# Optimization experiments

Hardware: AMD Instinct MI355X
Metric: run time of the kernel (lower is better)

The kernel has to match this reference:

```python
import jax, jax.numpy as jnp
import numpy as np

B, IN_F, OUT_F = 4096, 4096, 11008  # tokens, in_features, out_features


def setup_inputs() -> dict:
    key = jax.random.key(0)
    k1, k2, k3, k4 = jax.random.split(key, 4)
    x = jax.random.normal(k1, (B, IN_F), dtype=jnp.float32)
    # Each int holds two packed 4-bit codes (low nibble = even col, high nibble = odd col).
    packed_weights = jax.random.randint(k2, (OUT_F, IN_F // 2), 0, 256, dtype=jnp.int32)
    scales = jax.random.uniform(k3, (OUT_F,), dtype=jnp.float32) * 0.02 + 1e-4
    zero_points = jax.random.uniform(k4, (OUT_F,), dtype=jnp.float32) * 15.0
    return {"x": x, "packed_weights": packed_weights, "scales": scales,
            "zero_points": zero_points}


def _dequantize(packed_weights, scales, zero_points):
    # Unpack two 4-bit codes per byte -> q: [OUT_F, IN_F]
    low = (packed_weights & 15).astype(jnp.float32)
    high = ((packed_weights >> 4) & 15).astype(jnp.float32)
    q = jnp.stack([low, high], axis=-1).reshape(packed_weights.shape[0], -1)
    # Per-row affine dequant: w = (q - zero_point) * scale
    return (q - zero_points[:, None]) * scales[:, None]


def reference(x, packed_weights, scales, zero_points):
    W = _dequantize(packed_weights, scales, zero_points)  # [OUT_F, IN_F]
    return x @ W.T  # [B, OUT_F]
```

## Files before the change

kernel.cpp:

```cpp
#include <hip/hip_runtime.h>
#include <hip/hip_bf16.h>
#include <stdint.h>

#define M_DIM 4096
#define N_DIM 11008
#define K_DIM 4096
#define KP    (K_DIM / 2)

typedef __attribute__((ext_vector_type(4))) int i32x4;

#define AS1 __attribute__((address_space(1)))
#define AS3 __attribute__((address_space(3)))

__global__ __launch_bounds__(256) void pack_q(const int* __restrict__ pw,
                                              signed char* __restrict__ wq) {
  const int total = (N_DIM * KP) / 4;
  for (int i = blockIdx.x * 256 + threadIdx.x; i < total; i += gridDim.x * 256) {
    int4 p = ((const int4*)pw)[i];
    int v[4] = {p.x, p.y, p.z, p.w};
    unsigned int u0 = 0, u1 = 0;
#pragma unroll
    for (int j = 0; j < 2; ++j) {
      unsigned int b0 = (unsigned int)(2 * (v[j] & 15) - 15) & 0xFF;
      unsigned int b1 = (unsigned int)(2 * ((v[j] >> 4) & 15) - 15) & 0xFF;
      u0 |= (b0 | (b1 << 8)) << (16 * j);
    }
#pragma unroll
    for (int j = 0; j < 2; ++j) {
      unsigned int b0 = (unsigned int)(2 * (v[2 + j] & 15) - 15) & 0xFF;
      unsigned int b1 = (unsigned int)(2 * ((v[2 + j] >> 4) & 15) - 15) & 0xFF;
      u1 |= (b0 | (b1 << 8)) << (16 * j);
    }
    uint2 st; st.x = u0; st.y = u1;
    ((uint2*)wq)[i] = st;
  }
}

__global__ __launch_bounds__(256) void quant_x(const float* __restrict__ x,
                                               signed char* __restrict__ xq,
                                               float* __restrict__ r,
                                               float* __restrict__ sx) {
  const int row = blockIdx.x;
  const int t = threadIdx.x;
  const int lane = t & 63, wid = t >> 6;
  const float4* x4 = (const float4*)(x + (size_t)row * K_DIM);
  float4 v[4];
  float am = 0.0f, sm = 0.0f;
#pragma unroll
  for (int i = 0; i < 4; ++i) {
    v[i] = x4[i * 256 + t];
    sm += v[i].x + v[i].y + v[i].z + v[i].w;
    am = fmaxf(am, fmaxf(fmaxf(fabsf(v[i].x), fabsf(v[i].y)),
                         fmaxf(fabsf(v[i].z), fabsf(v[i].w))));
  }
#pragma unroll
  for (int off = 32; off >= 1; off >>= 1) {
    am = fmaxf(am, __shfl_xor(am, off));
    sm += __shfl_xor(sm, off);
  }
  __shared__ float smax[4], ssum[4];
  if (lane == 0) { smax[wid] = am; ssum[wid] = sm; }
  __syncthreads();
  am = fmaxf(fmaxf(smax[0], smax[1]), fmaxf(smax[2], smax[3]));
  sm = ssum[0] + ssum[1] + ssum[2] + ssum[3];
  const float inv = am > 0.0f ? 127.0f / am : 0.0f;
  unsigned int* xo = (unsigned int*)(xq + (size_t)row * K_DIM);
#pragma unroll
  for (int i = 0; i < 4; ++i) {
    int q0 = min(127, max(-127, __float2int_rn(v[i].x * inv)));
    int q1 = min(127, max(-127, __float2int_rn(v[i].y * inv)));
    int q2 = min(127, max(-127, __float2int_rn(v[i].z * inv)));
    int q3 = min(127, max(-127, __float2int_rn(v[i].w * inv)));
    xo[i * 256 + t] = ((unsigned int)q0 & 0xFF) | (((unsigned int)q1 & 0xFF) << 8) |
                      (((unsigned int)q2 & 0xFF) << 16) | (((unsigned int)q3 & 0xFF) << 24);
  }
  if (t == 0) { r[row] = sm; sx[row] = am > 0.0f ? am / 127.0f : 0.0f; }
}

#define BM 256
#define BN 256
#define BK 128
#define NTILE (K_DIM / BK)
#define NT_M (M_DIM / BM)
#define NT_N (N_DIM / BN)
#define NWG  (NT_M * NT_N)
#define HS 16384
#define PS 65536

#define WAITV(n) asm volatile("s_waitcnt vmcnt(" #n ")" ::: "memory")
#define WAITL0   asm volatile("s_waitcnt lgkmcnt(0)" ::: "memory")
#define BARR     do { asm volatile("" ::: "memory"); __builtin_amdgcn_s_barrier(); asm volatile("" ::: "memory"); } while (0)

__global__ __launch_bounds__(512, 2) void gemm_i8(const signed char* __restrict__ Xq,
                                                  const signed char* __restrict__ Wq,
                                                  const float* __restrict__ sc,
                                                  const float* __restrict__ zp,
                                                  const float* __restrict__ rbuf,
                                                  const float* __restrict__ sxbuf,
                                                  float* __restrict__ C) {
  __shared__ __align__(16) unsigned char lds8[131072];

  const int t = threadIdx.x;
  const int bid = blockIdx.x;
  const int swz = (bid & 7) * (NWG / 8) + (bid >> 3);
  const int tm = swz & 15;
  const int tn = swz >> 4;

  const int srow = t >> 3;
  const int g0 = (t & 7) ^ (srow & 7);
  const int koff = g0 * 16;
  const signed char* pB0c0 = Wq + (size_t)(tn * BN + srow) * K_DIM + koff;
  const signed char* pB0c1 = Wq + (size_t)(tn * BN + 64 + srow) * K_DIM + koff;
  const signed char* pB1c0 = Wq + (size_t)(tn * BN + 128 + srow) * K_DIM + koff;
  const signed char* pB1c1 = Wq + (size_t)(tn * BN + 192 + srow) * K_DIM + koff;
  const signed char* pA0c0 = Xq + (size_t)(tm * BM + srow) * K_DIM + koff;
  const signed char* pA0c1 = Xq + (size_t)(tm * BM + 64 + srow) * K_DIM + koff;
  const signed char* pA1c0 = Xq + (size_t)(tm * BM + 128 + srow) * K_DIM + koff;
  const signed char* pA1c1 = Xq + (size_t)(tm * BM + 192 + srow) * K_DIM + koff;
  const int d0 = t * 16;
  const int d1 = d0 + 8192;

  const int lane = t & 63;
  const int w = t >> 6;
  const int wm = w >> 2;
  const int wn = w & 3;
  const int lr = lane & 15, lk = lane >> 4;

  const int j0 = lk ^ (lr & 7);
  const int aB0 = (2 + wm) * HS + lr * 128 + j0 * 16;
  const int aB1 = aB0 ^ 64;
  const int bB0 = (wn >> 1) * HS + (wn & 1) * 8192 + lr * 128 + j0 * 16;
  const int bB1 = bB0 ^ 64;

  i32x4 acc[8][4] = {};

#define GLL(src, dstoff) \
  __builtin_amdgcn_global_load_lds((const AS1 void*)(src), (AS3 void*)(lds8 + (dstoff)), 16, 0, 0)

  GLL(pB0c0, 0 * HS + d0); GLL(pB0c1, 0 * HS + d1);
  GLL(pB1c0, 1 * HS + d0); GLL(pB1c1, 1 * HS + d1);
  GLL(pA0c0, 2 * HS + d0); GLL(pA0c1, 2 * HS + d1);
  GLL(pA1c0, 3 * HS + d0); GLL(pA1c1, 3 * HS + d1);
  GLL(pB0c0 + BK, 4 * HS + d0); GLL(pB0c1 + BK, 4 * HS + d1);
  GLL(pB1c0 + BK, 5 * HS + d0); GLL(pB1c1 + BK, 5 * HS + d1);
  pB0c0 += 2 * BK; pB0c1 += 2 * BK; pB1c0 += 2 * BK; pB1c1 += 2 * BK;
  pA0c0 += BK;     pA0c1 += BK;     pA1c0 += BK;     pA1c1 += BK;
  WAITV(4);
  BARR;

#define TILE(P, SA, SB, VMODE) do {                                                        \
    i32x4 af[4], bf0[4], bf1[4];                                                           \
                               \
    _Pragma("unroll") for (int i = 0; i < 4; ++i)                                          \
      af[i] = *(const i32x4*)(lds8 + (P) * PS + aB0 + i * 2048);                           \
    _Pragma("unroll") for (int n = 0; n < 4; ++n)                                          \
      bf0[n] = *(const i32x4*)(lds8 + (P) * PS + bB0 + n * 2048);                          \
    if (SA) { GLL(pA0c0, (((P) ^ 1) * 4 + 2) * HS + d0);                                   \
              GLL(pA0c1, (((P) ^ 1) * 4 + 2) * HS + d1);                                   \
              pA0c0 += BK; pA0c1 += BK; }                                                  \
    __builtin_amdgcn_s_setprio(1);                                                         \
    _Pragma("unroll") for (int i = 0; i < 4; ++i)                                          \
      _Pragma("unroll") for (int n = 0; n < 4; ++n)                                        \
        acc[i][n] = __builtin_amdgcn_mfma_i32_16x16x64_i8(af[i], bf0[n], acc[i][n], 0, 0, 0); \
    __builtin_amdgcn_s_setprio(0);                                                         \
      \
    _Pragma("unroll") for (int i = 0; i < 4; ++i)                                          \
      af[i] = *(const i32x4*)(lds8 + (P) * PS + aB0 + (4 + i) * 2048);                     \
    _Pragma("unroll") for (int n = 0; n < 4; ++n)                                          \
      bf1[n] = *(const i32x4*)(lds8 + (P) * PS + bB1 + n * 2048);                          \
    if (SA) { GLL(pA1c0, (((P) ^ 1) * 4 + 3) * HS + d0);                                   \
              GLL(pA1c1, (((P) ^ 1) * 4 + 3) * HS + d1);                                   \
              pA1c0 += BK; pA1c1 += BK; }                                                  \
    __builtin_amdgcn_s_setprio(1);                                                         \
    _Pragma("unroll") for (int i = 0; i < 4; ++i)                                          \
      _Pragma("unroll") for (int n = 0; n < 4; ++n)                                        \
        acc[4 + i][n] = __builtin_amdgcn_mfma_i32_16x16x64_i8(af[i], bf0[n], acc[4 + i][n], 0, 0, 0); \
    __builtin_amdgcn_s_setprio(0);                                                         \
    WAITL0;                                                                                \
    BARR;                                                                                  \
                                  \
    _Pragma("unroll") for (int i = 0; i < 4; ++i)                                          \
      af[i] = *(const i32x4*)(lds8 + (P) * PS + aB1 + i * 2048);                           \
    if (SB) { GLL(pB0c0, ((P) * 4 + 0) * HS + d0);                                         \
              GLL(pB0c1, ((P) * 4 + 0) * HS + d1);                                         \
              pB0c0 += BK; pB0c1 += BK; }                                                  \
    __builtin_amdgcn_s_setprio(1);                                                         \
    _Pragma("unroll") for (int i = 0; i < 4; ++i)                                          \
      _Pragma("unroll") for (int n = 0; n < 4; ++n)                                        \
        acc[i][n] = __builtin_amdgcn_mfma_i32_16x16x64_i8(af[i], bf1[n], acc[i][n], 0, 0, 0); \
    __builtin_amdgcn_s_setprio(0);                                                         \
              \
    _Pragma("unroll") for (int i = 0; i < 4; ++i)                                          \
      af[i] = *(const i32x4*)(lds8 + (P) * PS + aB1 + (4 + i) * 2048);                     \
    if (SB) { GLL(pB1c0, ((P) * 4 + 1) * HS + d0);                                         \
              GLL(pB1c1, ((P) * 4 + 1) * HS + d1);                                         \
              pB1c0 += BK; pB1c1 += BK; }                                                  \
    __builtin_amdgcn_s_setprio(1);                                                         \
    _Pragma("unroll") for (int i = 0; i < 4; ++i)                                          \
      _Pragma("unroll") for (int n = 0; n < 4; ++n)                                        \
        acc[4 + i][n] = __builtin_amdgcn_mfma_i32_16x16x64_i8(af[i], bf1[n], acc[4 + i][n], 0, 0, 0); \
    __builtin_amdgcn_s_setprio(0);                                                         \
    if ((VMODE) == 0) { WAITV(4); } else if ((VMODE) == 1) { WAITV(0); }                   \
    BARR;                                                                                  \
  } while (0)

  for (int it = 0; it < (NTILE - 2) / 2; ++it) {
    TILE(0, 1, 1, 0);
    TILE(1, 1, 1, 0);
  }
  TILE(0, 1, 0, 1);
  TILE(1, 0, 0, 2);

#undef TILE
#undef GLL

  const int row0 = tm * BM + wm * 128 + lk * 4;
  const int col0 = tn * BN + wn * 64 + lr;
  float sv[4], zv[4];
#pragma unroll
  for (int n = 0; n < 4; ++n) {
    sv[n] = sc[col0 + n * 16];
    zv[n] = 7.5f - zp[col0 + n * 16];
  }
#pragma unroll
  for (int m = 0; m < 8; ++m)
#pragma unroll
    for (int rr = 0; rr < 4; ++rr) {
      const int row = row0 + m * 16 + rr;
      const float rv = rbuf[row];
      const float hx = 0.5f * sxbuf[row];
#pragma unroll
      for (int n = 0; n < 4; ++n)
        C[(size_t)row * N_DIM + col0 + n * 16] = sv[n] * (hx * (float)acc[m][n][rr] + zv[n] * rv);
    }
}

__global__ __launch_bounds__(256) void fallback_gemm(const float* __restrict__ x,
                                                     const int* __restrict__ pw,
                                                     const float* __restrict__ sc,
                                                     const float* __restrict__ zp,
                                                     float* __restrict__ out) {
  __shared__ float Xs[64][33];
  __shared__ float Ws[64][33];
  const int bid = blockIdx.x;
  const int bm = bid & 63;
  const int bn = bid >> 6;
  const int t = threadIdx.x;
  const int tx = t & 15, ty = t >> 4;
  float acc[4][4] = {};
  for (int k0 = 0; k0 < K_DIM; k0 += 32) {
    __syncthreads();
#pragma unroll
    for (int i = 0; i < 8; ++i) {
      int e = t + i * 256; int r = e >> 5, c = e & 31;
      Xs[r][c] = x[(size_t)(bm * 64 + r) * K_DIM + k0 + c];
    }
#pragma unroll
    for (int i = 0; i < 4; ++i) {
      int e = t + i * 256; int rr = e >> 4, jj = e & 15;
      int row = bn * 64 + rr;
      int v = pw[(size_t)row * KP + (k0 >> 1) + jj];
      float s = sc[row], z = zp[row];
      Ws[rr][2 * jj]     = ((float)(v & 15) - z) * s;
      Ws[rr][2 * jj + 1] = ((float)((v >> 4) & 15) - z) * s;
    }
    __syncthreads();
#pragma unroll
    for (int kk = 0; kk < 32; ++kk) {
      float a[4], b[4];
#pragma unroll
      for (int i2 = 0; i2 < 4; ++i2) a[i2] = Xs[ty * 4 + i2][kk];
#pragma unroll
      for (int j2 = 0; j2 < 4; ++j2) b[j2] = Ws[tx * 4 + j2][kk];
#pragma unroll
      for (int i2 = 0; i2 < 4; ++i2)
#pragma unroll
        for (int j2 = 0; j2 < 4; ++j2) acc[i2][j2] += a[i2] * b[j2];
    }
  }
#pragma unroll
  for (int i2 = 0; i2 < 4; ++i2)
#pragma unroll
    for (int j2 = 0; j2 < 4; ++j2)
      out[(size_t)(bm * 64 + ty * 4 + i2) * N_DIM + bn * 64 + tx * 4 + j2] = acc[i2][j2];
}

extern "C" void kernel_launch(void* const* d_in, const int* in_sizes, int n_in,
                              void* d_out, int out_size, void* d_ws, size_t ws_size,
                              hipStream_t stream) {
  const float* x  = (const float*)d_in[0];
  const int*   pw = (const int*)d_in[1];
  const float* sc = (const float*)d_in[2];
  const float* zp = (const float*)d_in[3];
  float* out = (float*)d_out;

  const size_t wq_b = (size_t)N_DIM * K_DIM;
  const size_t xq_b = (size_t)M_DIM * K_DIM;
  const size_t need = wq_b + xq_b + 2 * 4096 * sizeof(float);

  if (ws_size >= need) {
    signed char* wq = (signed char*)d_ws;
    signed char* xq = wq + wq_b;
    float* rbuf  = (float*)((char*)d_ws + wq_b + xq_b);
    float* sxbuf = rbuf + 4096;
    hipLaunchKernelGGL(pack_q,  dim3(2048), dim3(256), 0, stream, pw, wq);
    hipLaunchKernelGGL(quant_x, dim3(4096), dim3(256), 0, stream, x, xq, rbuf, sxbuf);
    hipLaunchKernelGGL(gemm_i8, dim3(NWG),  dim3(512), 0, stream, xq, wq, sc, zp, rbuf, sxbuf, out);
  } else {
    hipLaunchKernelGGL(fallback_gemm, dim3(64 * 172), dim3(256), 0, stream, x, pw, sc, zp, out);
  }
}
```

Before: 225.2 us.

## Shrink GEMM tiles to 256x128x64 with triple-buffered LDS and fuse prep kernels

Merges the weight-repack and activation-quantize kernels into one launch, splitting the grid into two block ranges. Restructures the int8 MFMA GEMM from 256x256x128 double-buffered tiles to 256x128x64 tiles with a three-stage LDS ring, a new XOR swizzle and a simpler single-phase tile body. The goal is higher occupancy (launch bounds raised to 4 and a smaller LDS footprint) and deeper load pipelining. The cost is lower arithmetic intensity per tile, more global traffic for A, and twice as many workgroups.

```diff
diff --git a/kernel.cpp b/kernel.cpp
--- a/kernel.cpp
+++ b/kernel.cpp
@@ -12,93 +12,95 @@
 #define AS1 __attribute__((address_space(1)))
 #define AS3 __attribute__((address_space(3)))
 
-__global__ __launch_bounds__(256) void pack_q(const int* __restrict__ pw,
-                                              signed char* __restrict__ wq) {
-  const int total = (N_DIM * KP) / 4;
-  for (int i = blockIdx.x * 256 + threadIdx.x; i < total; i += gridDim.x * 256) {
-    int4 p = ((const int4*)pw)[i];
-    int v[4] = {p.x, p.y, p.z, p.w};
-    unsigned int u0 = 0, u1 = 0;
-#pragma unroll
-    for (int j = 0; j < 2; ++j) {
-      unsigned int b0 = (unsigned int)(2 * (v[j] & 15) - 15) & 0xFF;
-      unsigned int b1 = (unsigned int)(2 * ((v[j] >> 4) & 15) - 15) & 0xFF;
-      u0 |= (b0 | (b1 << 8)) << (16 * j);
-    }
-#pragma unroll
-    for (int j = 0; j < 2; ++j) {
-      unsigned int b0 = (unsigned int)(2 * (v[2 + j] & 15) - 15) & 0xFF;
-      unsigned int b1 = (unsigned int)(2 * ((v[2 + j] >> 4) & 15) - 15) & 0xFF;
-      u1 |= (b0 | (b1 << 8)) << (16 * j);
-    }
-    uint2 st; st.x = u0; st.y = u1;
-    ((uint2*)wq)[i] = st;
-  }
-}
-
-__global__ __launch_bounds__(256) void quant_x(const float* __restrict__ x,
-                                               signed char* __restrict__ xq,
-                                               float* __restrict__ r,
-                                               float* __restrict__ sx) {
-  const int row = blockIdx.x;
+__global__ __launch_bounds__(256) void prep(const float* __restrict__ x,
+                                            const int* __restrict__ pw,
+                                            signed char* __restrict__ xq,
+                                            signed char* __restrict__ wq,
+                                            float* __restrict__ r,
+                                            float* __restrict__ sx) {
+  const int b = blockIdx.x;
   const int t = threadIdx.x;
-  const int lane = t & 63, wid = t >> 6;
-  const float4* x4 = (const float4*)(x + (size_t)row * K_DIM);
-  float4 v[4];
-  float am = 0.0f, sm = 0.0f;
-#pragma unroll
-  for (int i = 0; i < 4; ++i) {
-    v[i] = x4[i * 256 + t];
-    sm += v[i].x + v[i].y + v[i].z + v[i].w;
-    am = fmaxf(am, fmaxf(fmaxf(fabsf(v[i].x), fabsf(v[i].y)),
-                         fmaxf(fabsf(v[i].z), fabsf(v[i].w))));
-  }
-#pragma unroll
-  for (int off = 32; off >= 1; off >>= 1) {
-    am = fmaxf(am, __shfl_xor(am, off));
-    sm += __shfl_xor(sm, off);
-  }
-  __shared__ float smax[4], ssum[4];
-  if (lane == 0) { smax[wid] = am; ssum[wid] = sm; }
-  __syncthreads();
-  am = fmaxf(fmaxf(smax[0], smax[1]), fmaxf(smax[2], smax[3]));
-  sm = ssum[0] + ssum[1] + ssum[2] + ssum[3];
-  const float inv = am > 0.0f ? 127.0f / am : 0.0f;
-  unsigned int* xo = (unsigned int*)(xq + (size_t)row * K_DIM);
-#pragma unroll
-  for (int i = 0; i < 4; ++i) {
-    int q0 = min(127, max(-127, __float2int_rn(v[i].x * inv)));
-    int q1 = min(127, max(-127, __float2int_rn(v[i].y * inv)));
-    int q2 = min(127, max(-127, __float2int_rn(v[i].z * inv)));
-    int q3 = min(127, max(-127, __float2int_rn(v[i].w * inv)));
-    xo[i * 256 + t] = ((unsigned int)q0 & 0xFF) | (((unsigned int)q1 & 0xFF) << 8) |
-                      (((unsigned int)q2 & 0xFF) << 16) | (((unsigned int)q3 & 0xFF) << 24);
-  }
-  if (t == 0) { r[row] = sm; sx[row] = am > 0.0f ? am / 127.0f : 0.0f; }
+  if (b < 4096) {
+    const int row = b;
+    const int lane = t & 63, wid = t >> 6;
+    const float4* x4 = (const float4*)(x + (size_t)row * K_DIM);
+    float4 v[4];
+    float am = 0.0f, sm = 0.0f;
+#pragma unroll
+    for (int i = 0; i < 4; ++i) {
+      v[i] = x4[i * 256 + t];
+      sm += v[i].x + v[i].y + v[i].z + v[i].w;
+      am = fmaxf(am, fmaxf(fmaxf(fabsf(v[i].x), fabsf(v[i].y)),
+                           fmaxf(fabsf(v[i].z), fabsf(v[i].w))));
+    }
+#pragma unroll
+    for (int off = 32; off >= 1; off >>= 1) {
+      am = fmaxf(am, __shfl_xor(am, off));
+      sm += __shfl_xor(sm, off);
+    }
+    __shared__ float smax[4], ssum[4];
+    if (lane == 0) { smax[wid] = am; ssum[wid] = sm; }
+    __syncthreads();
+    am = fmaxf(fmaxf(smax[0], smax[1]), fmaxf(smax[2], smax[3]));
+    sm = ssum[0] + ssum[1] + ssum[2] + ssum[3];
+    const float inv = am > 0.0f ? 127.0f / am : 0.0f;
+    unsigned int* xo = (unsigned int*)(xq + (size_t)row * K_DIM);
+#pragma unroll
+    for (int i = 0; i < 4; ++i) {
+      int q0 = min(127, max(-127, __float2int_rn(v[i].x * inv)));
+      int q1 = min(127, max(-127, __float2int_rn(v[i].y * inv)));
+      int q2 = min(127, max(-127, __float2int_rn(v[i].z * inv)));
+      int q3 = min(127, max(-127, __float2int_rn(v[i].w * inv)));
+      xo[i * 256 + t] = ((unsigned int)q0 & 0xFF) | (((unsigned int)q1 & 0xFF) << 8) |
+                        (((unsigned int)q2 & 0xFF) << 16) | (((unsigned int)q3 & 0xFF) << 24);
+    }
+    if (t == 0) { r[row] = sm; sx[row] = am > 0.0f ? am / 127.0f : 0.0f; }
+  } else {
+    const int total = (N_DIM * KP) / 4;
+    for (int i = (b - 4096) * 256 + t; i < total; i += 2048 * 256) {
+      int4 p = ((const int4*)pw)[i];
+      int v[4] = {p.x, p.y, p.z, p.w};
+      unsigned int u0 = 0, u1 = 0;
+#pragma unroll
+      for (int j = 0; j < 2; ++j) {
+        unsigned int b0 = (unsigned int)(2 * (v[j] & 15) - 15) & 0xFF;
+        unsigned int b1 = (unsigned int)(2 * ((v[j] >> 4) & 15) - 15) & 0xFF;
+        u0 |= (b0 | (b1 << 8)) << (16 * j);
+      }
+#pragma unroll
+      for (int j = 0; j < 2; ++j) {
+        unsigned int b0 = (unsigned int)(2 * (v[2 + j] & 15) - 15) & 0xFF;
+        unsigned int b1 = (unsigned int)(2 * ((v[2 + j] >> 4) & 15) - 15) & 0xFF;
+        u1 |= (b0 | (b1 << 8)) << (16 * j);
+      }
+      uint2 st; st.x = u0; st.y = u1;
+      ((uint2*)wq)[i] = st;
+    }
+  }
 }
 
 #define BM 256
-#define BN 256
-#define BK 128
+#define BN 128
+#define BK 64
 #define NTILE (K_DIM / BK)
 #define NT_M (M_DIM / BM)
 #define NT_N (N_DIM / BN)
 #define NWG  (NT_M * NT_N)
-#define HS 16384
-#define PS 65536
+#define SLOT 8192
+#define PAR  24576
 
 #define WAITV(n) asm volatile("s_waitcnt vmcnt(" #n ")" ::: "memory")
 #define WAITL0   asm volatile("s_waitcnt lgkmcnt(0)" ::: "memory")
 #define BARR     do { asm volatile("" ::: "memory"); __builtin_amdgcn_s_barrier(); asm volatile("" ::: "memory"); } while (0)
 
-__global__ __launch_bounds__(512, 2) void gemm_i8(const signed char* __restrict__ Xq,
+__global__ __launch_bounds__(512, 4) void gemm_i8(const signed char* __restrict__ Xq,
                                                   const signed char* __restrict__ Wq,
                                                   const float* __restrict__ sc,
                                                   const float* __restrict__ zp,
                                                   const float* __restrict__ rbuf,
                                                   const float* __restrict__ sxbuf,
                                                   float* __restrict__ C) {
-  __shared__ __align__(16) unsigned char lds8[131072];
+  __shared__ __align__(16) unsigned char lds8[73728];
 
   const int t = threadIdx.x;
   const int bid = blockIdx.x;
@@ -106,115 +108,76 @@
   const int tm = swz & 15;
   const int tn = swz >> 4;
 
-  const int srow = t >> 3;
-  const int g0 = (t & 7) ^ (srow & 7);
+  const int srow = t >> 2;
+  const int g0 = (t & 3) ^ (srow & 3) ^ ((srow >> 2) & 3);
   const int koff = g0 * 16;
-  const signed char* pB0c0 = Wq + (size_t)(tn * BN + srow) * K_DIM + koff;
-  const signed char* pB0c1 = Wq + (size_t)(tn * BN + 64 + srow) * K_DIM + koff;
-  const signed char* pB1c0 = Wq + (size_t)(tn * BN + 128 + srow) * K_DIM + koff;
-  const signed char* pB1c1 = Wq + (size_t)(tn * BN + 192 + srow) * K_DIM + koff;
-  const signed char* pA0c0 = Xq + (size_t)(tm * BM + srow) * K_DIM + koff;
-  const signed char* pA0c1 = Xq + (size_t)(tm * BM + 64 + srow) * K_DIM + koff;
-  const signed char* pA1c0 = Xq + (size_t)(tm * BM + 128 + srow) * K_DIM + koff;
-  const signed char* pA1c1 = Xq + (size_t)(tm * BM + 192 + srow) * K_DIM + koff;
-  const int d0 = t * 16;
-  const int d1 = d0 + 8192;
+  const signed char* pB  = Wq + (size_t)(tn * BN + srow) * K_DIM + koff;
+  const signed char* pA0 = Xq + (size_t)(tm * BM + srow) * K_DIM + koff;
+  const signed char* pA1 = Xq + (size_t)(tm * BM + 128 + srow) * K_DIM + koff;
+  const int d = t * 16;
 
   const int lane = t & 63;
   const int w = t >> 6;
-  const int wm = w >> 2;
-  const int wn = w & 3;
+  const int wm = w >> 1;
+  const int wn = w & 1;
   const int lr = lane & 15, lk = lane >> 4;
 
-  const int j0 = lk ^ (lr & 7);
-  const int aB0 = (2 + wm) * HS + lr * 128 + j0 * 16;
-  const int aB1 = aB0 ^ 64;
-  const int bB0 = (wn >> 1) * HS + (wn & 1) * 8192 + lr * 128 + j0 * 16;
-  const int bB1 = bB0 ^ 64;
-
-  i32x4 acc[8][4] = {};
+  const int js = lk ^ (lr & 3) ^ ((lr >> 2) & 3);
+  const int aBase = (1 + (wm >> 1)) * SLOT + ((wm & 1) * 64 + lr) * 64 + js * 16;
+  const int bBase = (wn * 64 + lr) * 64 + js * 16;
+
+  i32x4 acc[4][4] = {};
 
 #define GLL(src, dstoff) \
   __builtin_amdgcn_global_load_lds((const AS1 void*)(src), (AS3 void*)(lds8 + (dstoff)), 16, 0, 0)
 
-  GLL(pB0c0, 0 * HS + d0); GLL(pB0c1, 0 * HS + d1);
-  GLL(pB1c0, 1 * HS + d0); GLL(pB1c1, 1 * HS + d1);
-  GLL(pA0c0, 2 * HS + d0); GLL(pA0c1, 2 * HS + d1);
-  GLL(pA1c0, 3 * HS + d0); GLL(pA1c1, 3 * HS + d1);
-  GLL(pB0c0 + BK, 4 * HS + d0); GLL(pB0c1 + BK, 4 * HS + d1);
-  GLL(pB1c0 + BK, 5 * HS + d0); GLL(pB1c1 + BK, 5 * HS + d1);
-  pB0c0 += 2 * BK; pB0c1 += 2 * BK; pB1c0 += 2 * BK; pB1c1 += 2 * BK;
-  pA0c0 += BK;     pA0c1 += BK;     pA1c0 += BK;     pA1c1 += BK;
-  WAITV(4);
+  GLL(pB,            0 * PAR + 0 * SLOT + d);
+  GLL(pA0,           0 * PAR + 1 * SLOT + d);
+  GLL(pA1,           0 * PAR + 2 * SLOT + d);
+  GLL(pB  + BK,      1 * PAR + 0 * SLOT + d);
+  GLL(pA0 + BK,      1 * PAR + 1 * SLOT + d);
+  GLL(pA1 + BK,      1 * PAR + 2 * SLOT + d);
+  pB += 2 * BK; pA0 += 2 * BK; pA1 += 2 * BK;
+  WAITV(3);
   BARR;
 
-#define TILE(P, SA, SB, VMODE) do {                                                        \
-    i32x4 af[4], bf0[4], bf1[4];                                                           \
-                               \
+#define TILE(P, SS, VMODE) do {                                                            \
+    i32x4 af[4], bf[4];                                                                    \
     _Pragma("unroll") for (int i = 0; i < 4; ++i)                                          \
-      af[i] = *(const i32x4*)(lds8 + (P) * PS + aB0 + i * 2048);                           \
+      af[i] = *(const i32x4*)(lds8 + (P) * PAR + aBase + i * 1024);                        \
     _Pragma("unroll") for (int n = 0; n < 4; ++n)                                          \
-      bf0[n] = *(const i32x4*)(lds8 + (P) * PS + bB0 + n * 2048);                          \
-    if (SA) { GLL(pA0c0, (((P) ^ 1) * 4 + 2) * HS + d0);                                   \
-              GLL(pA0c1, (((P) ^ 1) * 4 + 2) * HS + d1);                                   \
-              pA0c0 += BK; pA0c1 += BK; }                                                  \
+      bf[n] = *(const i32x4*)(lds8 + (P) * PAR + bBase + n * 1024);                        \
+    if (SS) {                                                                              \
+      const int sp = ((P) + 2) % 3;                                                        \
+      GLL(pB,  sp * PAR + 0 * SLOT + d);                                                   \
+      GLL(pA0, sp * PAR + 1 * SLOT + d);                                                   \
+      GLL(pA1, sp * PAR + 2 * SLOT + d);                                                   \
+      pB += BK; pA0 += BK; pA1 += BK;                                                      \
+    }                                                                                      \
     __builtin_amdgcn_s_setprio(1);                                                         \
     _Pragma("unroll") for (int i = 0; i < 4; ++i)                                          \
       _Pragma("unroll") for (int n = 0; n < 4; ++n)                                        \
-        acc[i][n] = __builtin_amdgcn_mfma_i32_16x16x64_i8(af[i], bf0[n], acc[i][n], 0, 0, 0); \
+        acc[i][n] = __builtin_amdgcn_mfma_i32_16x16x64_i8(af[i], bf[n], acc[i][n], 0, 0, 0); \
     __builtin_amdgcn_s_setprio(0);                                                         \
-      \
-    _Pragma("unroll") for (int i = 0; i < 4; ++i)                                          \
-      af[i] = *(const i32x4*)(lds8 + (P) * PS + aB0 + (4 + i) * 2048);                     \
-    _Pragma("unroll") for (int n = 0; n < 4; ++n)                                          \
-      bf1[n] = *(const i32x4*)(lds8 + (P) * PS + bB1 + n * 2048);                          \
-    if (SA) { GLL(pA1c0, (((P) ^ 1) * 4 + 3) * HS + d0);                                   \
-              GLL(pA1c1, (((P) ^ 1) * 4 + 3) * HS + d1);                                   \
-              pA1c0 += BK; pA1c1 += BK; }                                                  \
-    __builtin_amdgcn_s_setprio(1);                                                         \
-    _Pragma("unroll") for (int i = 0; i < 4; ++i)                                          \
-      _Pragma("unroll") for (int n = 0; n < 4; ++n)                                        \
-        acc[4 + i][n] = __builtin_amdgcn_mfma_i32_16x16x64_i8(af[i], bf0[n], acc[4 + i][n], 0, 0, 0); \
-    __builtin_amdgcn_s_setprio(0);                                                         \
-    WAITL0;                                                                                \
-    BARR;                                                                                  \
-                                  \
-    _Pragma("unroll") for (int i = 0; i < 4; ++i)                                          \
-      af[i] = *(const i32x4*)(lds8 + (P) * PS + aB1 + i * 2048);                           \
-    if (SB) { GLL(pB0c0, ((P) * 4 + 0) * HS + d0);                                         \
-              GLL(pB0c1, ((P) * 4 + 0) * HS + d1);                                         \
-              pB0c0 += BK; pB0c1 += BK; }                                                  \
-    __builtin_amdgcn_s_setprio(1);                                                         \
-    _Pragma("unroll") for (int i = 0; i < 4; ++i)                                          \
-      _Pragma("unroll") for (int n = 0; n < 4; ++n)                                        \
-        acc[i][n] = __builtin_amdgcn_mfma_i32_16x16x64_i8(af[i], bf1[n], acc[i][n], 0, 0, 0); \
-    __builtin_amdgcn_s_setprio(0);                                                         \
-              \
-    _Pragma("unroll") for (int i = 0; i < 4; ++i)                                          \
-      af[i] = *(const i32x4*)(lds8 + (P) * PS + aB1 + (4 + i) * 2048);                     \
-    if (SB) { GLL(pB1c0, ((P) * 4 + 1) * HS + d0);                                         \
-              GLL(pB1c1, ((P) * 4 + 1) * HS + d1);                                         \
-              pB1c0 += BK; pB1c1 += BK; }                                                  \
-    __builtin_amdgcn_s_setprio(1);                                                         \
-    _Pragma("unroll") for (int i = 0; i < 4; ++i)                                          \
-      _Pragma("unroll") for (int n = 0; n < 4; ++n)                                        \
-        acc[4 + i][n] = __builtin_amdgcn_mfma_i32_16x16x64_i8(af[i], bf1[n], acc[4 + i][n], 0, 0, 0); \
-    __builtin_amdgcn_s_setprio(0);                                                         \
-    if ((VMODE) == 0) { WAITV(4); } else if ((VMODE) == 1) { WAITV(0); }                   \
+    WAITL0;          \
+    if ((VMODE) == 0) { WAITV(3); } else if ((VMODE) == 1) { WAITV(0); }                   \
     BARR;                                                                                  \
   } while (0)
 
-  for (int it = 0; it < (NTILE - 2) / 2; ++it) {
-    TILE(0, 1, 1, 0);
-    TILE(1, 1, 1, 0);
-  }
-  TILE(0, 1, 0, 1);
-  TILE(1, 0, 0, 2);
+  for (int it = 0; it < 20; ++it) {
+    TILE(0, 1, 0);
+    TILE(1, 1, 0);
+    TILE(2, 1, 0);
+  }
+  TILE(0, 1, 0);
+  TILE(1, 1, 0);
+  TILE(2, 0, 1);
+  TILE(0, 0, 2);
 
 #undef TILE
 #undef GLL
 
-  const int row0 = tm * BM + wm * 128 + lk * 4;
+  const int row0 = tm * BM + wm * 64 + lk * 4;
   const int col0 = tn * BN + wn * 64 + lr;
   float sv[4], zv[4];
 #pragma unroll
@@ -223,15 +186,15 @@
     zv[n] = 7.5f - zp[col0 + n * 16];
   }
 #pragma unroll
-  for (int m = 0; m < 8; ++m)
+  for (int i = 0; i < 4; ++i)
 #pragma unroll
     for (int rr = 0; rr < 4; ++rr) {
-      const int row = row0 + m * 16 + rr;
+      const int row = row0 + i * 16 + rr;
       const float rv = rbuf[row];
       const float hx = 0.5f * sxbuf[row];
 #pragma unroll
       for (int n = 0; n < 4; ++n)
-        C[(size_t)row * N_DIM + col0 + n * 16] = sv[n] * (hx * (float)acc[m][n][rr] + zv[n] * rv);
+        C[(size_t)row * N_DIM + col0 + n * 16] = sv[n] * (hx * (float)acc[i][n][rr] + zv[n] * rv);
     }
 }
 
@@ -252,8 +215,8 @@
     __syncthreads();
 #pragma unroll
     for (int i = 0; i < 8; ++i) {
-      int e = t + i * 256; int r = e >> 5, c = e & 31;
-      Xs[r][c] = x[(size_t)(bm * 64 + r) * K_DIM + k0 + c];
+      int e = t + i * 256; int rr = e >> 5, c = e & 31;
+      Xs[rr][c] = x[(size_t)(bm * 64 + rr) * K_DIM + k0 + c];
     }
 #pragma unroll
     for (int i = 0; i < 4; ++i) {
@@ -303,9 +266,8 @@
     signed char* xq = wq + wq_b;
     float* rbuf  = (float*)((char*)d_ws + wq_b + xq_b);
     float* sxbuf = rbuf + 4096;
-    hipLaunchKernelGGL(pack_q,  dim3(2048), dim3(256), 0, stream, pw, wq);
-    hipLaunchKernelGGL(quant_x, dim3(4096), dim3(256), 0, stream, x, xq, rbuf, sxbuf);
-    hipLaunchKernelGGL(gemm_i8, dim3(NWG),  dim3(512), 0, stream, xq, wq, sc, zp, rbuf, sxbuf, out);
+    hipLaunchKernelGGL(prep,    dim3(4096 + 2048), dim3(256), 0, stream, x, pw, xq, wq, rbuf, sxbuf);
+    hipLaunchKernelGGL(gemm_i8, dim3(NWG),         dim3(512), 0, stream, xq, wq, sc, zp, rbuf, sxbuf, out);
   } else {
     hipLaunchKernelGGL(fallback_gemm, dim3(64 * 172), dim3(256), 0, stream, x, pw, sc, zp, out);
   }
```

New measurement: 260.7 us. +15.8%, slower.
